# Optimization experiments

Measured on AMD Instinct MI355X. Metric: run time of the kernel, lower is better.

Reference implementation:

```python
import jax, jax.numpy as jnp
import numpy as np

N_EMBD = 2048
N_HEAD = 32
N_KV_HEADS = 8
HEAD_DIM = 64
N_REP = N_HEAD // N_KV_HEADS
MAX_SEQ_LEN = 4096
ROPE_THETA = 10000.0


def _precompute_freqs_cis(dim, end, theta=ROPE_THETA):
    freqs = 1.0 / theta ** (jnp.arange(0, dim, 2)[: dim // 2].astype(jnp.float32) / dim)
    t = jnp.arange(end, dtype=jnp.float32)
    freqs = jnp.outer(t, freqs)  # (end, dim//2)
    return jnp.cos(freqs), jnp.sin(freqs)


def setup_inputs() -> dict:
    key = jax.random.key(0)
    ks = jax.random.split(key, 5)
    B, S = 2, 2048
    x = jax.random.normal(ks[0], (B, S, N_EMBD), dtype=jnp.float32)
    # torch Linear(in, out, bias=False): y = x @ W.T, W is (out, in). We store (in, out).
    sc = 1.0 / np.sqrt(N_EMBD)
    wq = jax.random.normal(ks[1], (N_EMBD, N_EMBD), dtype=jnp.float32) * sc
    wk = jax.random.normal(ks[2], (N_EMBD, N_KV_HEADS * HEAD_DIM), dtype=jnp.float32) * sc
    wv = jax.random.normal(ks[3], (N_EMBD, N_KV_HEADS * HEAD_DIM), dtype=jnp.float32) * sc
    wo = jax.random.normal(ks[4], (N_EMBD, N_EMBD), dtype=jnp.float32) * sc
    freqs_cos, freqs_sin = _precompute_freqs_cis(HEAD_DIM, MAX_SEQ_LEN)
    return {"x": x, "wq": wq, "wk": wk, "wv": wv, "wo": wo,
            "freqs_cos": freqs_cos, "freqs_sin": freqs_sin}


def _apply_rotary(t, cos, sin):
    # t: (B, S, H, HD); interleaved real/imag pairs along last dim.
    shp = t.shape
    t2 = t.reshape(*shp[:-1], HEAD_DIM // 2, 2)
    r, i = t2[..., 0], t2[..., 1]
    out_r = r * cos - i * sin
    out_i = r * sin + i * cos
    return jnp.stack([out_r, out_i], axis=-1).reshape(shp)


def reference(x, wq, wk, wv, wo, freqs_cos, freqs_sin):
    B, S, _ = x.shape
    xq = (x @ wq).reshape(B, S, N_HEAD, HEAD_DIM)
    xk = (x @ wk).reshape(B, S, N_KV_HEADS, HEAD_DIM)
    xv = (x @ wv).reshape(B, S, N_KV_HEADS, HEAD_DIM)

    cos = freqs_cos[:S][None, :, None, :]  # (1, S, 1, HD/2)
    sin = freqs_sin[:S][None, :, None, :]
    xq = _apply_rotary(xq, cos, sin)
    xk = _apply_rotary(xk, cos, sin)

    # GQA: repeat KV heads (repeat_interleave along head dim)
    keys = jnp.repeat(xk, N_REP, axis=2)    # (B, S, H, HD)
    values = jnp.repeat(xv, N_REP, axis=2)

    scores = jnp.einsum('bqhd,bkhd->bhqk', xq, keys) / np.sqrt(HEAD_DIM)
    causal = jnp.tril(jnp.ones((S, S), dtype=bool))
    scores = jnp.where(causal, scores, -jnp.inf)
    probs = jax.nn.softmax(scores.astype(jnp.float32), axis=-1).astype(xq.dtype)
    out = jnp.einsum('bhqk,bkhd->bqhd', probs, values)  # (B, S, H, HD)
    out = out.reshape(B, S, N_EMBD)
    return out @ wo
```

## Files before the change

kernel.cpp:

```cpp
#include <hip/hip_runtime.h>
#include <hip/hip_fp16.h>
#include <stdint.h>

typedef _Float16 f16x8 __attribute__((ext_vector_type(8)));
typedef _Float16 f16x4 __attribute__((ext_vector_type(4)));
typedef _Float16 f16x2 __attribute__((ext_vector_type(2)));
typedef float f32x4 __attribute__((ext_vector_type(4)));
typedef float f32x16 __attribute__((ext_vector_type(16)));

#define B_ 2
#define S_ 2048
#define NE 2048
#define NH 32
#define NKV 8
#define HD 64
#define NTOK (B_ * S_)
#define QKVN 3072

__device__ __forceinline__ f16x2 pk(float a, float b) {
  return __builtin_bit_cast(f16x2, __builtin_amdgcn_cvt_pkrtz(a, b));
}

__device__ __forceinline__ void gld_lds16(void* lds, const void* g) {
  __builtin_amdgcn_global_load_lds(
      (const __attribute__((address_space(1))) void*)g,
      (__attribute__((address_space(3))) void*)lds, 16, 0, 0);
}

#define PREP_CONV 16384
__global__ __launch_bounds__(256) void prep_kernel(
    const float* __restrict__ x, _Float16* __restrict__ xb,
    const float* __restrict__ wq, const float* __restrict__ wk,
    const float* __restrict__ wv, const float* __restrict__ wo,
    _Float16* __restrict__ wqkv_t, _Float16* __restrict__ wo_t) {
  const int bid = blockIdx.x;
  const int tid = threadIdx.x;
  if (bid < PREP_CONV) {
    int i = bid * 256 + tid;
    float2 v = ((const float2*)x)[i];
    f16x2 h;
    h.x = (_Float16)v.x;
    h.y = (_Float16)v.y;
    ((f16x2*)xb)[i] = h;
    return;
  }
  __shared__ float tile[32][33];
  int r = bid - PREP_CONV;
  const float* src;
  _Float16* dst;
  int srcN, rowoff, bx, by;
  if (r < 4096) {
    src = wq; dst = wqkv_t; srcN = 2048; rowoff = 0;
    bx = r & 63; by = r >> 6;
  } else if (r < 5120) {
    r -= 4096;
    src = wk; dst = wqkv_t; srcN = 512; rowoff = 2048;
    bx = r & 15; by = r >> 4;
  } else if (r < 6144) {
    r -= 5120;
    src = wv; dst = wqkv_t; srcN = 512; rowoff = 2560;
    bx = r & 15; by = r >> 4;
  } else {
    r -= 6144;
    src = wo; dst = wo_t; srcN = 2048; rowoff = 0;
    bx = r & 63; by = r >> 6;
  }
  const int n0 = bx * 32, k0 = by * 32;
  const int tx = tid & 31, ty = tid >> 5;
  for (int i = ty; i < 32; i += 8)
    tile[i][tx] = src[(size_t)(k0 + i) * srcN + n0 + tx];
  __syncthreads();
  for (int i = ty; i < 32; i += 8)
    dst[(size_t)(rowoff + n0 + i) * 2048 + k0 + tx] = (_Float16)tile[tx][i];
}

template <int OUT_F32>
__global__ __launch_bounds__(256, 2) void gemm_bt(
    const _Float16* __restrict__ A, const _Float16* __restrict__ Bt,
    void* __restrict__ Cout, int M, int N, int K) {
  __shared__ _Float16 As[128 * 32];
  __shared__ _Float16 Bs[128 * 32];
  const int tid = threadIdx.x;
  const int wave = tid >> 6, lane = tid & 63;
  const int qd = lane >> 4, ln = lane & 15;
  const int m0 = blockIdx.y * 128, n0 = blockIdx.x * 128;
  const int wm = (wave >> 1) * 64, wn = (wave & 1) * 64;

  f32x4 acc[4][4] = {};

  const int srow = (lane >> 2);
  const int scol = (lane & 3) * 8;

  for (int k0 = 0; k0 < K; k0 += 32) {
    __syncthreads();
#pragma unroll
    for (int it = 0; it < 2; ++it) {
      int r = wave * 32 + it * 16 + srow;
      gld_lds16(&As[(wave * 32 + it * 16) * 32],
                A + (size_t)(m0 + r) * K + k0 + scol);
      gld_lds16(&Bs[(wave * 32 + it * 16) * 32],
                Bt + (size_t)(n0 + r) * K + k0 + scol);
    }
    __syncthreads();
    f16x8 a[4], b[4];
#pragma unroll
    for (int mt = 0; mt < 4; ++mt)
      a[mt] = *(const f16x8*)&As[(wm + mt * 16 + ln) * 32 + qd * 8];
#pragma unroll
    for (int nt = 0; nt < 4; ++nt)
      b[nt] = *(const f16x8*)&Bs[(wn + nt * 16 + ln) * 32 + qd * 8];
#pragma unroll
    for (int mt = 0; mt < 4; ++mt)
#pragma unroll
      for (int nt = 0; nt < 4; ++nt)
        acc[mt][nt] =
            __builtin_amdgcn_mfma_f32_16x16x32_f16(a[mt], b[nt], acc[mt][nt], 0, 0, 0);
  }

#pragma unroll
  for (int mt = 0; mt < 4; ++mt) {
    int row = m0 + wm + mt * 16 + qd * 4;
#pragma unroll
    for (int nt = 0; nt < 4; ++nt) {
      int col = n0 + wn + nt * 16 + ln;
#pragma unroll
      for (int r = 0; r < 4; ++r) {
        if (OUT_F32)
          ((float*)Cout)[(size_t)(row + r) * N + col] = acc[mt][nt][r];
        else
          ((_Float16*)Cout)[(size_t)(row + r) * N + col] =
              (_Float16)acc[mt][nt][r];
      }
    }
  }
}

#define ROPE_BLKS 20480
__global__ __launch_bounds__(256) void rope_vtrans_kernel(
    const _Float16* __restrict__ qkv, const float* __restrict__ fcos,
    const float* __restrict__ fsin, _Float16* __restrict__ Qb,
    _Float16* __restrict__ Kb, _Float16* __restrict__ Vtg) {
  const int tid = threadIdx.x;
  if (blockIdx.x < ROPE_BLKS) {
    const float QSC = 0.125f * 1.44269504088896f;
    int idx = blockIdx.x * 256 + tid;
    int t = idx / 1280;
    int col = (idx - t * 1280) * 2;
    int b = t >> 11, s = t & 2047;
    float v0 = (float)qkv[(size_t)t * QKVN + col];
    float v1 = (float)qkv[(size_t)t * QKVN + col + 1];
    _Float16* dst;
    size_t off;
    int d;
    float sc;
    if (col < 2048) {
      int h = col >> 6;
      d = col & 63;
      dst = Qb;
      off = ((size_t)(b * NH + h) * S_ + s) * HD + d;
      sc = QSC;
    } else {
      int cc = col - 2048;
      int h = cc >> 6;
      d = cc & 63;
      dst = Kb;
      off = ((size_t)(b * NKV + h) * S_ + s) * HD + d;
      sc = 1.0f;
    }
    float c = fcos[s * 32 + (d >> 1)], sn = fsin[s * 32 + (d >> 1)];
    f16x2 o;
    o.x = (_Float16)((v0 * c - v1 * sn) * sc);
    o.y = (_Float16)((v0 * sn + v1 * c) * sc);
    *(f16x2*)(dst + off) = o;
    return;
  }
  __shared__ _Float16 tile[64][65];
  int r = blockIdx.x - ROPE_BLKS;
  int t0 = (r & 31) * 64;
  int kv = (r >> 5) & 7, b = r >> 8;
  for (int slot = tid; slot < 4096; slot += 256) {
    int rr = slot >> 6, c = slot & 63;
    tile[rr][c] = qkv[(size_t)(b * S_ + t0 + rr) * QKVN + 2560 + kv * 64 + c];
  }
  __syncthreads();
  size_t base = ((size_t)(b * NKV + kv) * HD) * S_;
  for (int slot = tid; slot < 4096; slot += 256) {
    int d = slot >> 6, rr = slot & 63;
    Vtg[base + (size_t)d * S_ + t0 + rr] = tile[rr][d];
  }
}

__global__ __launch_bounds__(128, 2) void attn_kernel(
    const _Float16* __restrict__ Qb, const _Float16* __restrict__ Kb,
    const _Float16* __restrict__ Vtg, _Float16* __restrict__ Ob) {
  constexpr float M_SHIFT = 10.0f;
  __shared__ _Float16 Ks[64 * 64];
  __shared__ _Float16 Vs[64 * 64];
  const int tid = threadIdx.x;
  const int wave = tid >> 6, lane = tid & 63;
  const int mrow = lane & 31;
  const bool half = (lane >> 5) != 0;
  const int h = blockIdx.y, b = blockIdx.z;
  const int kvh = h >> 2;

  const _Float16* Qh = Qb + ((size_t)(b * NH + h) * S_) * HD;
  const _Float16* Kh = Kb + ((size_t)(b * NKV + kvh) * S_) * HD;
  const _Float16* Vh = Vtg + ((size_t)(b * NKV + kvh) * HD) * S_;

  const int sr = tid >> 3;
  const int scc = tid & 7;
  const int swz = (scc ^ (sr & 7)) * 8;

#pragma unroll
  for (int pass = 0; pass < 2; ++pass) {
    const int qt = pass ? blockIdx.x : (31 - blockIdx.x);
    const int q0 = qt * 64;
    const int nkt = qt + 1;

    const int qrow = q0 + wave * 32 + mrow;
    f16x8 aq[4];
#pragma unroll
    for (int kk = 0; kk < 4; ++kk)
      aq[kk] = *(const f16x8*)(Qh + (size_t)qrow * HD + kk * 16 +
                               (half ? 8 : 0));

    f32x16 accO[2] = {};
    float lsum = 0.f;

    f16x8 kp[4], vp[4];
#pragma unroll
    for (int i = 0; i < 4; ++i) {
      kp[i] = *(const f16x8*)(Kh + (size_t)(sr + i * 16) * HD + scc * 8);
      vp[i] = *(const f16x8*)(Vh + (size_t)(sr + i * 16) * S_ + scc * 8);
    }
#pragma unroll
    for (int i = 0; i < 4; ++i) {
      *(f16x8*)&Ks[(sr + i * 16) * 64 + swz] = kp[i];
      *(f16x8*)&Vs[(sr + i * 16) * 64 + swz] = vp[i];
    }

    for (int kt = 0; kt < nkt; ++kt) {
      __syncthreads();
      if (kt + 1 < nkt) {
#pragma unroll
        for (int i = 0; i < 4; ++i) {
          kp[i] = *(const f16x8*)(Kh +
                                  (size_t)((kt + 1) * 64 + sr + i * 16) * HD +
                                  scc * 8);
          vp[i] = *(const f16x8*)(Vh + (size_t)(sr + i * 16) * S_ +
                                  (kt + 1) * 64 + scc * 8);
        }
      }

      f32x16 s[2];
#pragma unroll
      for (int nt = 0; nt < 2; ++nt)
#pragma unroll
        for (int r = 0; r < 16; ++r) s[nt][r] = -M_SHIFT;
#pragma unroll
      for (int kk = 0; kk < 4; ++kk) {
        int c = kk * 2 + (half ? 1 : 0);
#pragma unroll
        for (int nt = 0; nt < 2; ++nt) {
          int krow = nt * 32 + mrow;
          f16x8 bk = *(const f16x8*)&Ks[krow * 64 + ((c ^ (krow & 7)) * 8)];
          s[nt] = __builtin_amdgcn_mfma_f32_32x32x16_f16(bk, aq[kk], s[nt],
                                                         0, 0, 0);
        }
      }

      const bool edge = (kt == nkt - 1);
      float pf[2][16];
#pragma unroll
      for (int nt = 0; nt < 2; ++nt)
#pragma unroll
        for (int r = 0; r < 16; ++r) {
          int key = kt * 64 + nt * 32 + (r & 3) + 8 * (r >> 2) +
                    (half ? 4 : 0);
          float p = exp2f(s[nt][r]);
          if (edge && key > qrow) p = 0.f;
          lsum += p;
          pf[nt][r] = p;
        }

      f16x2 P2[2][4][2];
#pragma unroll
      for (int nt = 0; nt < 2; ++nt)
#pragma unroll
        for (int c = 0; c < 4; ++c)
#pragma unroll
          for (int u = 0; u < 2; ++u)
            P2[nt][c][u] = pk(pf[nt][4 * c + 2 * u], pf[nt][4 * c + 2 * u + 1]);

#pragma unroll
      for (int s4 = 0; s4 < 4; ++s4) {
        const int ntp = s4 >> 1;
        const int gA = (2 * s4) & 3, gB = (2 * s4 + 1) & 3;
        f16x2 own0 = half ? P2[ntp][gB][0] : P2[ntp][gA][0];
        f16x2 own1 = half ? P2[ntp][gB][1] : P2[ntp][gA][1];
        f16x2 snd0 = half ? P2[ntp][gA][0] : P2[ntp][gB][0];
        f16x2 snd1 = half ? P2[ntp][gA][1] : P2[ntp][gB][1];
        f16x2 rcv0 = __builtin_bit_cast(
            f16x2, __shfl_xor(__builtin_bit_cast(int, snd0), 32));
        f16x2 rcv1 = __builtin_bit_cast(
            f16x2, __shfl_xor(__builtin_bit_cast(int, snd1), 32));
        union {
          f16x2 h2[4];
          f16x8 h8;
        } bp;
        bp.h2[0] = half ? rcv0 : own0;
        bp.h2[1] = half ? rcv1 : own1;
        bp.h2[2] = half ? own0 : rcv0;
        bp.h2[3] = half ? own1 : rcv1;
        const int c = 2 * s4 + (half ? 1 : 0);
#pragma unroll
        for (int ntd = 0; ntd < 2; ++ntd) {
          int drow = ntd * 32 + mrow;
          f16x8 bv = *(const f16x8*)&Vs[drow * 64 + ((c ^ (drow & 7)) * 8)];
          accO[ntd] = __builtin_amdgcn_mfma_f32_32x32x16_f16(bv, bp.h8,
                                                             accO[ntd], 0, 0, 0);
        }
      }

      __syncthreads();
      if (kt + 1 < nkt) {
#pragma unroll
        for (int i = 0; i < 4; ++i) {
          *(f16x8*)&Ks[(sr + i * 16) * 64 + swz] = kp[i];
          *(f16x8*)&Vs[(sr + i * 16) * 64 + swz] = vp[i];
        }
      }
    }

    float tot = lsum + __shfl_xor(lsum, 32);
    float inv = 1.f / tot;
    size_t base = ((size_t)(b * S_) + qrow) * NE + h * HD;
#pragma unroll
    for (int ntd = 0; ntd < 2; ++ntd)
#pragma unroll
      for (int rq = 0; rq < 4; ++rq) {
        int d0 = ntd * 32 + 8 * rq + (half ? 4 : 0);
        union {
          f16x2 h2[2];
          f16x4 h4;
        } o;
        o.h2[0] = pk(accO[ntd][4 * rq + 0] * inv, accO[ntd][4 * rq + 1] * inv);
        o.h2[1] = pk(accO[ntd][4 * rq + 2] * inv, accO[ntd][4 * rq + 3] * inv);
        *(f16x4*)(Ob + base + d0) = o.h4;
      }
  }
}

extern "C" void kernel_launch(void* const* d_in, const int* in_sizes, int n_in,
                              void* d_out, int out_size, void* d_ws,
                              size_t ws_size, hipStream_t stream) {
  const float* x = (const float*)d_in[0];
  const float* wq = (const float*)d_in[1];
  const float* wk = (const float*)d_in[2];
  const float* wv = (const float*)d_in[3];
  const float* wo = (const float*)d_in[4];
  const float* fcos = (const float*)d_in[5];
  const float* fsin = (const float*)d_in[6];

  char* ws = (char*)d_ws;
  _Float16* xb = (_Float16*)(ws);
  _Float16* wqkv_t = (_Float16*)(ws + 16777216);
  _Float16* wo_t = (_Float16*)(ws + 29360128);
  _Float16* qkv = (_Float16*)(ws + 37748736);
  _Float16* Qb = (_Float16*)(ws + 62914560);
  _Float16* Kb = (_Float16*)(ws + 79691776);
  _Float16* Vb = (_Float16*)(ws + 83886080);
  _Float16* Ob = (_Float16*)(ws + 88080384);

  prep_kernel<<<PREP_CONV + 10240, 256, 0, stream>>>(x, xb, wq, wk, wv, wo,
                                                     wqkv_t, wo_t);

  gemm_bt<0><<<dim3(QKVN / 128, NTOK / 128), 256, 0, stream>>>(
      xb, wqkv_t, qkv, NTOK, QKVN, NE);

  rope_vtrans_kernel<<<ROPE_BLKS + 512, 256, 0, stream>>>(qkv, fcos, fsin,
                                                          Qb, Kb, Vb);

  attn_kernel<<<dim3(16, NH, B_), 128, 0, stream>>>(Qb, Kb, Vb, Ob);

  gemm_bt<1><<<dim3(NE / 128, NTOK / 128), 256, 0, stream>>>(
      Ob, wo_t, d_out, NTOK, NE, NE);
}
```

Before: 320.6 us.

## Fuse RoPE and V transpose into QKV GEMM epilogue

```diff
diff --git a/kernel.cpp b/kernel.cpp
--- a/kernel.cpp
+++ b/kernel.cpp
@@ -135,58 +135,91 @@
   }
 }
 
-#define ROPE_BLKS 20480
-__global__ __launch_bounds__(256) void rope_vtrans_kernel(
-    const _Float16* __restrict__ qkv, const float* __restrict__ fcos,
-    const float* __restrict__ fsin, _Float16* __restrict__ Qb,
-    _Float16* __restrict__ Kb, _Float16* __restrict__ Vtg) {
+__global__ __launch_bounds__(256, 2) void gemm_qkv(
+    const _Float16* __restrict__ A, const _Float16* __restrict__ Bt,
+    const float* __restrict__ fcos, const float* __restrict__ fsin,
+    _Float16* __restrict__ Qb, _Float16* __restrict__ Kb,
+    _Float16* __restrict__ Vtg) {
+  const int K = NE;
+  __shared__ _Float16 As[128 * 32];
+  __shared__ _Float16 Bs[128 * 32];
   const int tid = threadIdx.x;
-  if (blockIdx.x < ROPE_BLKS) {
-    const float QSC = 0.125f * 1.44269504088896f;
-    int idx = blockIdx.x * 256 + tid;
-    int t = idx / 1280;
-    int col = (idx - t * 1280) * 2;
-    int b = t >> 11, s = t & 2047;
-    float v0 = (float)qkv[(size_t)t * QKVN + col];
-    float v1 = (float)qkv[(size_t)t * QKVN + col + 1];
-    _Float16* dst;
-    size_t off;
-    int d;
-    float sc;
-    if (col < 2048) {
-      int h = col >> 6;
-      d = col & 63;
-      dst = Qb;
-      off = ((size_t)(b * NH + h) * S_ + s) * HD + d;
-      sc = QSC;
-    } else {
-      int cc = col - 2048;
-      int h = cc >> 6;
-      d = cc & 63;
-      dst = Kb;
-      off = ((size_t)(b * NKV + h) * S_ + s) * HD + d;
-      sc = 1.0f;
-    }
-    float c = fcos[s * 32 + (d >> 1)], sn = fsin[s * 32 + (d >> 1)];
-    f16x2 o;
-    o.x = (_Float16)((v0 * c - v1 * sn) * sc);
-    o.y = (_Float16)((v0 * sn + v1 * c) * sc);
-    *(f16x2*)(dst + off) = o;
-    return;
-  }
-  __shared__ _Float16 tile[64][65];
-  int r = blockIdx.x - ROPE_BLKS;
-  int t0 = (r & 31) * 64;
-  int kv = (r >> 5) & 7, b = r >> 8;
-  for (int slot = tid; slot < 4096; slot += 256) {
-    int rr = slot >> 6, c = slot & 63;
-    tile[rr][c] = qkv[(size_t)(b * S_ + t0 + rr) * QKVN + 2560 + kv * 64 + c];
-  }
-  __syncthreads();
-  size_t base = ((size_t)(b * NKV + kv) * HD) * S_;
-  for (int slot = tid; slot < 4096; slot += 256) {
-    int d = slot >> 6, rr = slot & 63;
-    Vtg[base + (size_t)d * S_ + t0 + rr] = tile[rr][d];
+  const int wave = tid >> 6, lane = tid & 63;
+  const int qd = lane >> 4, ln = lane & 15;
+  const int m0 = blockIdx.y * 128, n0 = blockIdx.x * 128;
+  const int wm = (wave >> 1) * 64, wn = (wave & 1) * 64;
+
+  f32x4 acc[4][4] = {};
+
+  const int srow = (lane >> 2);
+  const int scol = (lane & 3) * 8;
+
+  for (int k0 = 0; k0 < K; k0 += 32) {
+    __syncthreads();
+#pragma unroll
+    for (int it = 0; it < 2; ++it) {
+      int r = wave * 32 + it * 16 + srow;
+      gld_lds16(&As[(wave * 32 + it * 16) * 32],
+                A + (size_t)(m0 + r) * K + k0 + scol);
+      gld_lds16(&Bs[(wave * 32 + it * 16) * 32],
+                Bt + (size_t)(n0 + r) * K + k0 + scol);
+    }
+    __syncthreads();
+    f16x8 a[4], b[4];
+#pragma unroll
+    for (int mt = 0; mt < 4; ++mt)
+      a[mt] = *(const f16x8*)&As[(wm + mt * 16 + ln) * 32 + qd * 8];
+#pragma unroll
+    for (int nt = 0; nt < 4; ++nt)
+      b[nt] = *(const f16x8*)&Bs[(wn + nt * 16 + ln) * 32 + qd * 8];
+#pragma unroll
+    for (int mt = 0; mt < 4; ++mt)
+#pragma unroll
+      for (int nt = 0; nt < 4; ++nt)
+        acc[mt][nt] =
+            __builtin_amdgcn_mfma_f32_16x16x32_f16(a[mt], b[nt], acc[mt][nt], 0, 0, 0);
+  }
+
+  const float QSC = 0.125f * 1.44269504088896f;
+  const bool isQ = (n0 < 2048);
+  const bool isV = (n0 >= 2560);
+  const float sgn = (ln & 1) ? 1.f : -1.f;
+
+#pragma unroll
+  for (int mt = 0; mt < 4; ++mt) {
+    int row0 = m0 + wm + mt * 16 + qd * 4;
+    int bb = row0 >> 11;
+    int s0 = row0 & 2047;
+#pragma unroll
+    for (int nt = 0; nt < 4; ++nt) {
+      int col = n0 + wn + nt * 16 + ln;
+      if (isV) {
+        int kv = (col - 2560) >> 6, d = col & 63;
+        union {
+          f16x2 h2[2];
+          f16x4 h4;
+        } o;
+        o.h2[0] = pk(acc[mt][nt][0], acc[mt][nt][1]);
+        o.h2[1] = pk(acc[mt][nt][2], acc[mt][nt][3]);
+        *(f16x4*)(Vtg + ((size_t)(bb * NKV + kv) * HD + d) * S_ + s0) = o.h4;
+      } else {
+        int d = col & 63;
+        int hh = isQ ? (col >> 6) : ((col - 2048) >> 6);
+        float sc = isQ ? QSC : 1.0f;
+        _Float16* dstp = isQ ? (Qb + ((size_t)(bb * NH + hh) * S_) * HD)
+                             : (Kb + ((size_t)(bb * NKV + hh) * S_) * HD);
+#pragma unroll
+        for (int r = 0; r < 4; ++r) {
+          int s = s0 + r;
+          float v = acc[mt][nt][r];
+          float t = __shfl_xor(v, 1);
+          float cc = fcos[s * 32 + (d >> 1)];
+          float sn = fsin[s * 32 + (d >> 1)];
+          float out = (cc * v + sgn * sn * t) * sc;
+          dstp[(size_t)s * HD + d] = (_Float16)out;
+        }
+      }
+    }
   }
 }
 
@@ -366,7 +399,6 @@
   _Float16* xb = (_Float16*)(ws);
   _Float16* wqkv_t = (_Float16*)(ws + 16777216);
   _Float16* wo_t = (_Float16*)(ws + 29360128);
-  _Float16* qkv = (_Float16*)(ws + 37748736);
   _Float16* Qb = (_Float16*)(ws + 62914560);
   _Float16* Kb = (_Float16*)(ws + 79691776);
   _Float16* Vb = (_Float16*)(ws + 83886080);
@@ -375,11 +407,8 @@
   prep_kernel<<<PREP_CONV + 10240, 256, 0, stream>>>(x, xb, wq, wk, wv, wo,
                                                      wqkv_t, wo_t);
 
-  gemm_bt<0><<<dim3(QKVN / 128, NTOK / 128), 256, 0, stream>>>(
-      xb, wqkv_t, qkv, NTOK, QKVN, NE);
-
-  rope_vtrans_kernel<<<ROPE_BLKS + 512, 256, 0, stream>>>(qkv, fcos, fsin,
-                                                          Qb, Kb, Vb);
+  gemm_qkv<<<dim3(QKVN / 128, NTOK / 128), 256, 0, stream>>>(
+      xb, wqkv_t, fcos, fsin, Qb, Kb, Vb);
 
   attn_kernel<<<dim3(16, NH, B_), 128, 0, stream>>>(Qb, Kb, Vb, Ob);
 
```

New measurement: 323.1 us. No clear change (+0.8%).
